# Kernel tuning notes

Hardware: AMD Instinct MI355X
Metric: run time of the kernel (lower is better)

Reference implementation:

```python
import jax, jax.numpy as jnp
import numpy as np

BS, N, E = 16, 1024, 262144
IN_DIM, HID, OUT, NREL, NBASES = 3072, 512, 128, 8, 4
N_LAYERS = 3


def setup_inputs() -> dict:
    key = jax.random.key(0)
    ks = jax.random.split(key, 10)
    tot = BS * N
    return {
        "h": jax.random.normal(ks[0], (BS, N, IN_DIM), jnp.float32),
        "src": jax.random.randint(ks[1], (E,), 0, tot, jnp.int32),
        "dst": jax.random.randint(ks[2], (E,), 0, tot, jnp.int32),
        "r": jax.random.randint(ks[3], (E,), 0, NREL, jnp.int32),
        "norm": jax.random.uniform(ks[4], (E,), jnp.float32),
        "W_elmo": jax.random.normal(ks[5], (IN_DIM, 256), jnp.float32) * 0.02,
        "b_elmo": jnp.zeros((256,), jnp.float32),
        "comp": jax.random.normal(ks[6], (NREL, NBASES), jnp.float32),
        "V": jax.random.normal(ks[7], (NBASES, HID, HID), jnp.float32) * 0.04,
        "b_gcn": jnp.zeros((HID,), jnp.float32),
        "W_out": jax.random.normal(ks[8], (HID, OUT), jnp.float32) * 0.04,
        "b_out": jnp.zeros((OUT,), jnp.float32),
    }


def reference(h, src, dst, r, norm, W_elmo, b_elmo, comp, V, b_gcn, W_out, b_out):
    bs, n, _ = h.shape
    tot = bs * n
    # elmo_fnn + relu, then concat with zeros -> gnn_h_dim = 512
    x = jax.nn.relu(h @ W_elmo + b_elmo)                 # [bs, N, 256]
    x = jnp.concatenate([x, jnp.zeros_like(x)], axis=-1)  # [bs, N, 512]
    x = x.reshape(tot, HID)                               # flattened batched-graph nodes

    coef = comp[r]  # [E, NBASES] per-edge relation coefficients (basis decomposition)
    nb = V.shape[0]
    for _ in range(N_LAYERS):  # shared RelGraphConv applied repeatedly
        hs = x[src]  # [E, HID] gather source node features per edge
        # message m_e = h_src @ (sum_b comp[r_e, b] * V_b); loop over small fixed basis count
        msg = coef[:, 0:1] * (hs @ V[0])
        for b in range(1, nb):
            msg = msg + coef[:, b:b + 1] * (hs @ V[b])
        msg = msg * norm[:, None]  # per-edge norm weighting
        x = jax.ops.segment_sum(msg, dst, num_segments=tot)  # scatter-aggregate to dst
        x = jax.nn.relu(x + b_gcn)  # bias + activation (no self-loop, dropout=0)

    x = x.reshape(bs, n, HID).mean(axis=1)  # mean over nodes per graph
    logits = x @ W_out + b_out
    return jax.nn.softmax(logits, axis=-1)
```

## Files before the change

kernel.cpp:

```cpp
#include <hip/hip_runtime.h>

typedef unsigned short u16;
typedef unsigned int   u32;
typedef u16   u16x4 __attribute__((ext_vector_type(4)));
typedef u16   u16x8 __attribute__((ext_vector_type(8)));
typedef short s16x8 __attribute__((ext_vector_type(8)));
typedef u32   u32x4 __attribute__((ext_vector_type(4)));
typedef float f32x4 __attribute__((ext_vector_type(4)));

__device__ __forceinline__ float bf2f(u16 u) {
    u32 x = ((u32)u) << 16;
    return __builtin_bit_cast(float, x);
}
__device__ __forceinline__ u16 f2bf(float f) {
    u32 u = __builtin_bit_cast(u32, f);
    u32 r = u + 0x7FFFu + ((u >> 16) & 1u);
    return (u16)(r >> 16);
}
__device__ __forceinline__ u32 cvtpk(float a, float b) {
    u32 r;
    asm("v_cvt_pk_bf16_f32 %0, %1, %2" : "=v"(r) : "v"(a), "v"(b));
    return r;
}

__device__ __forceinline__ void gload16(const void* g, void* lds) {
    __builtin_amdgcn_global_load_lds((const __attribute__((address_space(1))) void*)g,
                                     (__attribute__((address_space(3))) void*)lds, 16, 0, 0);
}

#define TOT   16384
#define HID   512
#define NRELS 8
#define EDGES 262144
#define INDIM 3072
#define NOUT  128
#define NGRAPH 16
#define NODESPER 1024
#define EKSPLIT 4

#define OFF_XB     ((size_t)0)
#define OFF_Y      (OFF_XB + 16777216)
#define OFF_WCT    (OFF_Y + 134217728)
#define OFF_WET    (OFF_WCT + 4194304)
#define OFF_CNT    (OFF_WET + 1572864)
#define OFF_ROWPTR (OFF_CNT + 65536)
#define OFF_CURSOR (OFF_ROWPTR + 65552)
#define OFF_EPK    (OFF_CURSOR + 65536)
#define OFF_ENORM  (OFF_EPK + 1048576)
#define OFF_PART   (OFF_ENORM + 1048576)

__global__ __launch_bounds__(256) void k_prep_wcat(const float* __restrict__ comp,
                                                   const float* __restrict__ V,
                                                   u16* __restrict__ WcatT) {
    __shared__ float tile[64][65];
    const int r = blockIdx.z, k0 = blockIdx.x * 64, n0 = blockIdx.y * 64;
    const float c0 = comp[r * 4], c1 = comp[r * 4 + 1], c2 = comp[r * 4 + 2], c3 = comp[r * 4 + 3];
    const int tn = threadIdx.x & 63;
    const int tk = threadIdx.x >> 6;
#pragma unroll
    for (int i = 0; i < 16; ++i) {
        int k = tk + i * 4;
        const float* vp = V + (size_t)(k0 + k) * 512 + n0 + tn;
        tile[k][tn] = c0 * vp[0] + c1 * vp[262144] + c2 * vp[2 * 262144] + c3 * vp[3 * 262144];
    }
    __syncthreads();
    const int kk = threadIdx.x & 63;
#pragma unroll
    for (int i = 0; i < 16; ++i) {
        int n = (threadIdx.x >> 6) + i * 4;
        WcatT[((size_t)(r * 512 + n0 + n) << 9) + k0 + kk] = f2bf(tile[kk][n]);
    }
}

__global__ __launch_bounds__(256) void k_prep_welmo(const float* __restrict__ W,
                                                    u16* __restrict__ WT) {
    __shared__ float tile[64][65];
    const int k0 = blockIdx.x * 64, n0 = blockIdx.y * 64;
    const int tn = threadIdx.x & 63;
    const int tk = threadIdx.x >> 6;
#pragma unroll
    for (int i = 0; i < 16; ++i) {
        int k = tk + i * 4;
        tile[k][tn] = W[(size_t)(k0 + k) * 256 + n0 + tn];
    }
    __syncthreads();
    const int kk = threadIdx.x & 63;
#pragma unroll
    for (int i = 0; i < 16; ++i) {
        int n = (threadIdx.x >> 6) + i * 4;
        WT[(size_t)(n0 + n) * 3072 + k0 + kk] = f2bf(tile[kk][n]);
    }
}

__global__ __launch_bounds__(256) void k_hist(const int* __restrict__ dst, int* __restrict__ cnt) {
    int e = blockIdx.x * 256 + threadIdx.x;
    atomicAdd(&cnt[dst[e]], 1);
}

__global__ __launch_bounds__(1024) void k_scan(const int* __restrict__ cnt,
                                               int* __restrict__ rowptr,
                                               int* __restrict__ cursor) {
    __shared__ int part[1024];
    int t = threadIdx.x;
    int loc[16];
    int s = 0;
    int base = t * 16;
#pragma unroll
    for (int i = 0; i < 16; ++i) { loc[i] = s; s += cnt[base + i]; }
    part[t] = s;
    __syncthreads();
    for (int off = 1; off < 1024; off <<= 1) {
        int v = (t >= off) ? part[t - off] : 0;
        __syncthreads();
        part[t] += v;
        __syncthreads();
    }
    int excl = (t == 0) ? 0 : part[t - 1];
#pragma unroll
    for (int i = 0; i < 16; ++i) {
        int v = excl + loc[i];
        rowptr[base + i] = v;
        cursor[base + i] = v;
    }
    if (t == 1023) rowptr[TOT] = part[1023];
}

__global__ __launch_bounds__(256) void k_scatter(const int* __restrict__ src,
                                                 const int* __restrict__ dst,
                                                 const int* __restrict__ rel,
                                                 const float* __restrict__ norm,
                                                 int* __restrict__ cursor,
                                                 int* __restrict__ epk,
                                                 float* __restrict__ enorm) {
    int e = blockIdx.x * 256 + threadIdx.x;
    int d = dst[e];
    int pos = atomicAdd(&cursor[d], 1);
    epk[pos] = (src[e] << 3) | rel[e];
    enorm[pos] = norm[e];
}

__global__ __launch_bounds__(256, 4) void k_gemm(const u16* __restrict__ A,
                                                 const u16* __restrict__ BT,
                                                 u16* __restrict__ C,
                                                 int K, int lda, int ldb, int ldc) {
    __shared__ __align__(16) u16 As[128 * 64];
    __shared__ __align__(16) u16 Bs[128 * 64];

    const int t = threadIdx.x;
    const int lin = blockIdx.y * 128 + blockIdx.x;
    const int swz = (lin & 7) * 512 + (lin >> 3);
    const int tileM = (swz & 127) * 128;
    const int tileN = (swz >> 7) * 128;

    const int w = t >> 6, l = t & 63;
    const int wr = w >> 1, wc = w & 1;
    const int lo = l & 15, hi = l >> 4;

    const int srow8 = l >> 3;
    const int scol = ((l & 7) ^ srow8) * 8;

    f32x4 acc[4][4];
#pragma unroll
    for (int m = 0; m < 4; ++m)
#pragma unroll
        for (int n = 0; n < 4; ++n) acc[m][n] = f32x4{0.f, 0.f, 0.f, 0.f};

    for (int k0 = 0; k0 < K; k0 += 64) {
#pragma unroll
        for (int i = 0; i < 4; ++i) {
            const int rowblk = (w * 4 + i) * 8;
            gload16(A + (size_t)(tileM + rowblk + srow8) * lda + k0 + scol, &As[rowblk * 64]);
            gload16(BT + (size_t)(tileN + rowblk + srow8) * ldb + k0 + scol, &Bs[rowblk * 64]);
        }
        __syncthreads();

#pragma unroll
        for (int kk = 0; kk < 2; ++kk) {
            s16x8 af[4], bf[4];
#pragma unroll
            for (int m = 0; m < 4; ++m) {
                int row = wr * 64 + m * 16 + lo;
                int boff = (row * 128 + kk * 64 + hi * 16) ^ ((row & 7) << 4);
                af[m] = *(const s16x8*)((const char*)As + boff);
            }
#pragma unroll
            for (int n = 0; n < 4; ++n) {
                int row = wc * 64 + n * 16 + lo;
                int boff = (row * 128 + kk * 64 + hi * 16) ^ ((row & 7) << 4);
                bf[n] = *(const s16x8*)((const char*)Bs + boff);
            }
#pragma unroll
            for (int m = 0; m < 4; ++m)
#pragma unroll
                for (int n = 0; n < 4; ++n)
                    acc[m][n] = __builtin_amdgcn_mfma_f32_16x16x32_bf16(
                        af[m], bf[n], acc[m][n], 0, 0, 0);
        }
        __syncthreads();
    }

#pragma unroll
    for (int m = 0; m < 4; ++m)
#pragma unroll
        for (int n = 0; n < 4; ++n) {
            int col = tileN + wc * 64 + n * 16 + lo;
#pragma unroll
            for (int j = 0; j < 4; ++j) {
                int row = tileM + wr * 64 + m * 16 + hi * 4 + j;
                C[(size_t)row * ldc + col] = f2bf(acc[m][n][j]);
            }
        }
}

__global__ __launch_bounds__(256, 2) void k_gemm_elmo(const float* __restrict__ A,
                                                      const u16* __restrict__ BT,
                                                      float* __restrict__ Cp) {
    __shared__ __align__(16) float As[128 * 64];
    __shared__ __align__(16) u16   Bs[256 * 64];

    const int t = threadIdx.x;
    const int tileM = blockIdx.x * 128;
    const int kz = blockIdx.y;
    const int kbeg = kz * (INDIM / EKSPLIT);

    const int w = t >> 6, l = t & 63;
    const int wr = w >> 1, wc = w & 1;
    const int lo = l & 15, hi = l >> 4;

    const int ar = l >> 4;
    const int br = l >> 3;
    const int bcol = ((l & 7) ^ br) * 8;

    f32x4 acc[4][8];
#pragma unroll
    for (int m = 0; m < 4; ++m)
#pragma unroll
        for (int n = 0; n < 8; ++n) acc[m][n] = f32x4{0.f, 0.f, 0.f, 0.f};

    for (int ks = 0; ks < 12; ++ks) {
        const int k0 = kbeg + ks * 64;
#pragma unroll
        for (int i = 0; i < 8; ++i) {
            const int RA = (w * 8 + i) * 4;
            const int ca = (l & 15) ^ ((RA & 15) + ar);
            gload16(A + (size_t)(tileM + RA + ar) * INDIM + k0 + ca * 4, &As[RA * 64]);
            const int RB = (w * 8 + i) * 8;
            gload16(BT + (size_t)(RB + br) * INDIM + k0 + bcol, &Bs[RB * 64]);
        }
        __syncthreads();

#pragma unroll
        for (int kk = 0; kk < 2; ++kk) {
            s16x8 afr[4], bfr[8];
#pragma unroll
            for (int m = 0; m < 4; ++m) {
                int ra = wr * 64 + m * 16 + lo;
                int x0 = kk * 8 + hi * 2;
                const char* base = (const char*)As + ra * 256;
                f32x4 p = *(const f32x4*)(base + (((x0) ^ (ra & 15)) << 4));
                f32x4 q = *(const f32x4*)(base + (((x0 + 1) ^ (ra & 15)) << 4));
                u32x4 pk = {cvtpk(p[0], p[1]), cvtpk(p[2], p[3]),
                            cvtpk(q[0], q[1]), cvtpk(q[2], q[3])};
                afr[m] = __builtin_bit_cast(s16x8, pk);
            }
#pragma unroll
            for (int n = 0; n < 8; ++n) {
                int rb = wc * 128 + n * 16 + lo;
                int boff = (rb * 128 + kk * 64 + hi * 16) ^ ((rb & 7) << 4);
                bfr[n] = *(const s16x8*)((const char*)Bs + boff);
            }
#pragma unroll
            for (int m = 0; m < 4; ++m)
#pragma unroll
                for (int n = 0; n < 8; ++n)
                    acc[m][n] = __builtin_amdgcn_mfma_f32_16x16x32_bf16(
                        afr[m], bfr[n], acc[m][n], 0, 0, 0);
        }
        __syncthreads();
    }

    float* cp = Cp + (size_t)kz * TOT * 256;
#pragma unroll
    for (int m = 0; m < 4; ++m)
#pragma unroll
        for (int n = 0; n < 8; ++n) {
            int col = wc * 128 + n * 16 + lo;
#pragma unroll
            for (int j = 0; j < 4; ++j) {
                int row = tileM + wr * 64 + m * 16 + hi * 4 + j;
                cp[(size_t)row * 256 + col] = acc[m][n][j];
            }
        }
}

__global__ __launch_bounds__(256) void k_elmo_reduce(const float* __restrict__ Cp,
                                                     const float* __restrict__ bias,
                                                     u16* __restrict__ xb) {
    int idx = blockIdx.x * 256 + threadIdx.x;
    int row = idx >> 6;
    int c4 = (idx & 63) * 4;
    f32x4 s = *(const f32x4*)(Cp + (size_t)row * 256 + c4);
#pragma unroll
    for (int p = 1; p < EKSPLIT; ++p)
        s += *(const f32x4*)(Cp + (size_t)p * TOT * 256 + (size_t)row * 256 + c4);
    f32x4 bv = *(const f32x4*)(bias + c4);
    u16x4 o;
#pragma unroll
    for (int j = 0; j < 4; ++j) o[j] = f2bf(fmaxf(s[j] + bv[j], 0.f));
    *(u16x4*)(xb + (size_t)row * HID + c4) = o;
}

__global__ __launch_bounds__(256) void k_agg(const u16* __restrict__ y,
                                             const int* __restrict__ rowptr,
                                             const int* __restrict__ epk,
                                             const float* __restrict__ enorm,
                                             const float* __restrict__ bgcn,
                                             u16* __restrict__ xout) {
    __shared__ int   s_epk[64];
    __shared__ float s_nrm[64];
    const int d = blockIdx.x, t = threadIdx.x;
    const u32* yw = (const u32*)y;

    float2 bv = *(const float2*)(bgcn + 2 * t);
    float a0 = bv.x, a1 = bv.y;

    const int beg = rowptr[d], end = rowptr[d + 1];
    for (int base = beg; base < end; base += 64) {
        const int m = min(64, end - base);
        if (t < m) { s_epk[t] = epk[base + t]; s_nrm[t] = enorm[base + t]; }
        __syncthreads();
        int c = 0;
        for (; c + 16 <= m; c += 16) {
            u32 wv[16];
            float nv[16];
#pragma unroll
            for (int q = 0; q < 16; ++q) {
                int k = s_epk[c + q];
                nv[q] = s_nrm[c + q];
                wv[q] = yw[((size_t)(k >> 3) << 11) + ((k & 7) << 8) + t];
            }
#pragma unroll
            for (int q = 0; q < 16; ++q) {
                a0 = fmaf(nv[q], bf2f((u16)wv[q]), a0);
                a1 = fmaf(nv[q], bf2f((u16)(wv[q] >> 16)), a1);
            }
        }
        for (; c + 4 <= m; c += 4) {
            u32 wv[4];
            float nv[4];
#pragma unroll
            for (int q = 0; q < 4; ++q) {
                int k = s_epk[c + q];
                nv[q] = s_nrm[c + q];
                wv[q] = yw[((size_t)(k >> 3) << 11) + ((k & 7) << 8) + t];
            }
#pragma unroll
            for (int q = 0; q < 4; ++q) {
                a0 = fmaf(nv[q], bf2f((u16)wv[q]), a0);
                a1 = fmaf(nv[q], bf2f((u16)(wv[q] >> 16)), a1);
            }
        }
        for (; c < m; ++c) {
            int k0 = s_epk[c];
            float n0 = s_nrm[c];
            u32 w0 = yw[((size_t)(k0 >> 3) << 11) + ((k0 & 7) << 8) + t];
            a0 = fmaf(n0, bf2f((u16)w0), a0);
            a1 = fmaf(n0, bf2f((u16)(w0 >> 16)), a1);
        }
        __syncthreads();
    }
    u32 o = (u32)f2bf(fmaxf(a0, 0.f)) | ((u32)f2bf(fmaxf(a1, 0.f)) << 16);
    ((u32*)xout)[((size_t)d << 8) + t] = o;
}

__global__ __launch_bounds__(512) void k_mean1(const u16* __restrict__ xb,
                                               float* __restrict__ part) {
    int g = blockIdx.x >> 4, chunk = blockIdx.x & 15, t = threadIdx.x;
    const u16* base = xb + ((size_t)g * NODESPER + chunk * 64) * HID;
    float s = 0.f;
    for (int n = 0; n < 64; ++n) s += bf2f(base[(size_t)n * HID + t]);
    part[(size_t)blockIdx.x * HID + t] = s;
}

__global__ __launch_bounds__(512) void k_final2(const float* __restrict__ part,
                                                const float* __restrict__ W_out,
                                                const float* __restrict__ b_out,
                                                float* __restrict__ out) {
    int g = blockIdx.x, t = threadIdx.x;
    __shared__ float mean_s[512];
    __shared__ float lg[128];
    __shared__ float red[128];
    float s = 0.f;
#pragma unroll
    for (int c = 0; c < 16; ++c) s += part[((size_t)g * 16 + c) * HID + t];
    mean_s[t] = s * (1.0f / (float)NODESPER);
    __syncthreads();
    if (t < NOUT) {
        float a = b_out[t];
        for (int k = 0; k < HID; ++k) a = fmaf(mean_s[k], W_out[(size_t)k * NOUT + t], a);
        lg[t] = a;
        red[t] = a;
    }
    __syncthreads();
    for (int off = 64; off > 0; off >>= 1) {
        if (t < off) red[t] = fmaxf(red[t], red[t + off]);
        __syncthreads();
    }
    float mx = red[0];
    __syncthreads();
    if (t < NOUT) { float e = expf(lg[t] - mx); lg[t] = e; red[t] = e; }
    __syncthreads();
    for (int off = 64; off > 0; off >>= 1) {
        if (t < off) red[t] += red[t + off];
        __syncthreads();
    }
    if (t < NOUT) out[(size_t)g * NOUT + t] = lg[t] / red[0];
}

extern "C" void kernel_launch(void* const* d_in, const int* in_sizes, int n_in,
                              void* d_out, int out_size, void* d_ws, size_t ws_size,
                              hipStream_t stream) {
    const float* h      = (const float*)d_in[0];
    const int*   src    = (const int*)d_in[1];
    const int*   dst    = (const int*)d_in[2];
    const int*   rel    = (const int*)d_in[3];
    const float* norm   = (const float*)d_in[4];
    const float* W_elmo = (const float*)d_in[5];
    const float* b_elmo = (const float*)d_in[6];
    const float* comp   = (const float*)d_in[7];
    const float* V      = (const float*)d_in[8];
    const float* b_gcn  = (const float*)d_in[9];
    const float* W_out  = (const float*)d_in[10];
    const float* b_out  = (const float*)d_in[11];
    float* out = (float*)d_out;

    char* ws = (char*)d_ws;
    u16*   xb     = (u16*)(ws + OFF_XB);
    u16*   y      = (u16*)(ws + OFF_Y);
    float* elmoP  = (float*)(ws + OFF_Y);
    u16*   wcatT  = (u16*)(ws + OFF_WCT);
    u16*   welmoT = (u16*)(ws + OFF_WET);
    int*   cnt    = (int*)(ws + OFF_CNT);
    int*   rowptr = (int*)(ws + OFF_ROWPTR);
    int*   cursor = (int*)(ws + OFF_CURSOR);
    int*   epk    = (int*)(ws + OFF_EPK);
    float* enorm  = (float*)(ws + OFF_ENORM);
    float* part   = (float*)(ws + OFF_PART);

    hipMemsetAsync(xb, 0, (size_t)TOT * HID * 2, stream);
    hipMemsetAsync(cnt, 0, (size_t)TOT * 4, stream);

    k_prep_wcat<<<dim3(8, 8, 8), 256, 0, stream>>>(comp, V, wcatT);
    k_prep_welmo<<<dim3(48, 4), 256, 0, stream>>>(W_elmo, welmoT);

    k_hist<<<EDGES / 256, 256, 0, stream>>>(dst, cnt);
    k_scan<<<1, 1024, 0, stream>>>(cnt, rowptr, cursor);
    k_scatter<<<EDGES / 256, 256, 0, stream>>>(src, dst, rel, norm, cursor, epk, enorm);

    k_gemm_elmo<<<dim3(128, EKSPLIT), 256, 0, stream>>>(h, welmoT, elmoP);
    k_elmo_reduce<<<4096, 256, 0, stream>>>(elmoP, b_elmo, xb);

    for (int L = 0; L < 3; ++L) {
        const int Keff = (L == 0) ? 256 : 512;
        k_gemm<<<dim3(128, 32), 256, 0, stream>>>(xb, wcatT, y, Keff, HID, HID,
                                                  NRELS * HID);
        k_agg<<<TOT, 256, 0, stream>>>(y, rowptr, epk, enorm, b_gcn, xb);
    }

    k_mean1<<<NGRAPH * 16, 512, 0, stream>>>(xb, part);
    k_final2<<<NGRAPH, 512, 0, stream>>>(part, W_out, b_out, out);
}
```

Baseline: 534.1 us.

## Triple-buffer GEMM K-loop and use wave-per-node vectorized aggregation

The relation GEMM now stages K in 32-wide slices across three LDS buffers, prefetching two slices ahead. It uses explicit vmcnt waits and a single barrier per step, and raises MFMA priority, so global loads overlap compute. The aggregation kernel maps one wavefront per destination node with 16-byte gathers per lane, replacing one block per node with LDS staging and block syncs. Occupancy bound drops from 4 to 3 blocks, and the per-node edge loop is now serial within a wave, with less memory-level parallelism per node.

Result: slower. 574.8 us (+7.6%).

```diff
diff --git a/kernel.cpp b/kernel.cpp
--- a/kernel.cpp
+++ b/kernel.cpp
@@ -139,12 +139,12 @@
     enorm[pos] = norm[e];
 }
 
-__global__ __launch_bounds__(256, 4) void k_gemm(const u16* __restrict__ A,
+__global__ __launch_bounds__(256, 3) void k_gemm(const u16* __restrict__ A,
                                                  const u16* __restrict__ BT,
                                                  u16* __restrict__ C,
                                                  int K, int lda, int ldb, int ldc) {
-    __shared__ __align__(16) u16 As[128 * 64];
-    __shared__ __align__(16) u16 Bs[128 * 64];
+    __shared__ __align__(16) u16 As[3][128 * 32];
+    __shared__ __align__(16) u16 Bs[3][128 * 32];
 
     const int t = threadIdx.x;
     const int lin = blockIdx.y * 128 + blockIdx.x;
@@ -156,8 +156,8 @@
     const int wr = w >> 1, wc = w & 1;
     const int lo = l & 15, hi = l >> 4;
 
-    const int srow8 = l >> 3;
-    const int scol = ((l & 7) ^ srow8) * 8;
+    const int sr = l >> 2;
+    const int sc = ((l & 3) ^ ((l >> 3) & 3)) * 8;
 
     f32x4 acc[4][4];
 #pragma unroll
@@ -165,39 +165,59 @@
 #pragma unroll
         for (int n = 0; n < 4; ++n) acc[m][n] = f32x4{0.f, 0.f, 0.f, 0.f};
 
-    for (int k0 = 0; k0 < K; k0 += 64) {
-#pragma unroll
-        for (int i = 0; i < 4; ++i) {
-            const int rowblk = (w * 4 + i) * 8;
-            gload16(A + (size_t)(tileM + rowblk + srow8) * lda + k0 + scol, &As[rowblk * 64]);
-            gload16(BT + (size_t)(tileN + rowblk + srow8) * ldb + k0 + scol, &Bs[rowblk * 64]);
-        }
-        __syncthreads();
-
-#pragma unroll
-        for (int kk = 0; kk < 2; ++kk) {
-            s16x8 af[4], bf[4];
-#pragma unroll
-            for (int m = 0; m < 4; ++m) {
-                int row = wr * 64 + m * 16 + lo;
-                int boff = (row * 128 + kk * 64 + hi * 16) ^ ((row & 7) << 4);
-                af[m] = *(const s16x8*)((const char*)As + boff);
-            }
-#pragma unroll
-            for (int n = 0; n < 4; ++n) {
-                int row = wc * 64 + n * 16 + lo;
-                int boff = (row * 128 + kk * 64 + hi * 16) ^ ((row & 7) << 4);
-                bf[n] = *(const s16x8*)((const char*)Bs + boff);
-            }
-#pragma unroll
-            for (int m = 0; m < 4; ++m)
-#pragma unroll
-                for (int n = 0; n < 4; ++n)
-                    acc[m][n] = __builtin_amdgcn_mfma_f32_16x16x32_bf16(
-                        af[m], bf[n], acc[m][n], 0, 0, 0);
-        }
-        __syncthreads();
-    }
+    const int nt = K >> 5;
+
+#define STG(pa, pb, ks)                                                              \
+    {                                                                                \
+        const int k0_ = (ks) * 32;                                                   \
+        _Pragma("unroll") for (int i = 0; i < 2; ++i) {                              \
+            const int rg = (w * 2 + i) * 16;                                         \
+            gload16(A + (size_t)(tileM + rg + sr) * lda + k0_ + sc, (pa) + rg * 32); \
+            gload16(BT + (size_t)(tileN + rg + sr) * ldb + k0_ + sc, (pb) + rg * 32);\
+        }                                                                            \
+    }
+
+    u16 *pa0 = &As[0][0], *pa1 = &As[1][0], *pa2 = &As[2][0];
+    u16 *pb0 = &Bs[0][0], *pb1 = &Bs[1][0], *pb2 = &Bs[2][0];
+
+    STG(pa0, pb0, 0);
+    STG(pa1, pb1, 1);
+
+    for (int tt = 0; tt < nt; ++tt) {
+        if (tt < nt - 1) asm volatile("s_waitcnt vmcnt(4)" ::: "memory");
+        else             asm volatile("s_waitcnt vmcnt(0)" ::: "memory");
+        __builtin_amdgcn_sched_barrier(0);
+        __builtin_amdgcn_s_barrier();
+        __builtin_amdgcn_sched_barrier(0);
+
+        if (tt + 2 < nt) STG(pa2, pb2, tt + 2);
+
+        const char* Ab = (const char*)pa0;
+        const char* Bb = (const char*)pb0;
+        s16x8 af[4], bf[4];
+#pragma unroll
+        for (int m = 0; m < 4; ++m) {
+            int ra = wr * 64 + m * 16 + lo;
+            af[m] = *(const s16x8*)(Ab + ra * 64 + ((hi ^ ((ra >> 1) & 3)) << 4));
+        }
+#pragma unroll
+        for (int n = 0; n < 4; ++n) {
+            int rb = wc * 64 + n * 16 + lo;
+            bf[n] = *(const s16x8*)(Bb + rb * 64 + ((hi ^ ((rb >> 1) & 3)) << 4));
+        }
+        __builtin_amdgcn_s_setprio(1);
+#pragma unroll
+        for (int m = 0; m < 4; ++m)
+#pragma unroll
+            for (int n = 0; n < 4; ++n)
+                acc[m][n] = __builtin_amdgcn_mfma_f32_16x16x32_bf16(
+                    af[m], bf[n], acc[m][n], 0, 0, 0);
+        __builtin_amdgcn_s_setprio(0);
+
+        u16* ta = pa0; pa0 = pa1; pa1 = pa2; pa2 = ta;
+        u16* tb = pb0; pb0 = pb1; pb1 = pb2; pb2 = tb;
+    }
+#undef STG
 
 #pragma unroll
     for (int m = 0; m < 4; ++m)
@@ -316,61 +336,54 @@
                                              const float* __restrict__ enorm,
                                              const float* __restrict__ bgcn,
                                              u16* __restrict__ xout) {
-    __shared__ int   s_epk[64];
-    __shared__ float s_nrm[64];
-    const int d = blockIdx.x, t = threadIdx.x;
-    const u32* yw = (const u32*)y;
-
-    float2 bv = *(const float2*)(bgcn + 2 * t);
-    float a0 = bv.x, a1 = bv.y;
-
-    const int beg = rowptr[d], end = rowptr[d + 1];
-    for (int base = beg; base < end; base += 64) {
-        const int m = min(64, end - base);
-        if (t < m) { s_epk[t] = epk[base + t]; s_nrm[t] = enorm[base + t]; }
-        __syncthreads();
-        int c = 0;
-        for (; c + 16 <= m; c += 16) {
-            u32 wv[16];
-            float nv[16];
-#pragma unroll
-            for (int q = 0; q < 16; ++q) {
-                int k = s_epk[c + q];
-                nv[q] = s_nrm[c + q];
-                wv[q] = yw[((size_t)(k >> 3) << 11) + ((k & 7) << 8) + t];
-            }
-#pragma unroll
-            for (int q = 0; q < 16; ++q) {
-                a0 = fmaf(nv[q], bf2f((u16)wv[q]), a0);
-                a1 = fmaf(nv[q], bf2f((u16)(wv[q] >> 16)), a1);
-            }
-        }
-        for (; c + 4 <= m; c += 4) {
-            u32 wv[4];
-            float nv[4];
-#pragma unroll
-            for (int q = 0; q < 4; ++q) {
-                int k = s_epk[c + q];
-                nv[q] = s_nrm[c + q];
-                wv[q] = yw[((size_t)(k >> 3) << 11) + ((k & 7) << 8) + t];
-            }
-#pragma unroll
-            for (int q = 0; q < 4; ++q) {
-                a0 = fmaf(nv[q], bf2f((u16)wv[q]), a0);
-                a1 = fmaf(nv[q], bf2f((u16)(wv[q] >> 16)), a1);
-            }
-        }
-        for (; c < m; ++c) {
-            int k0 = s_epk[c];
-            float n0 = s_nrm[c];
-            u32 w0 = yw[((size_t)(k0 >> 3) << 11) + ((k0 & 7) << 8) + t];
-            a0 = fmaf(n0, bf2f((u16)w0), a0);
-            a1 = fmaf(n0, bf2f((u16)(w0 >> 16)), a1);
-        }
-        __syncthreads();
-    }
-    u32 o = (u32)f2bf(fmaxf(a0, 0.f)) | ((u32)f2bf(fmaxf(a1, 0.f)) << 16);
-    ((u32*)xout)[((size_t)d << 8) + t] = o;
+    const int wid = (blockIdx.x * 256 + threadIdx.x) >> 6;
+    const int l = threadIdx.x & 63;
+    const u32x4* yv = (const u32x4*)y;
+
+    float a[8];
+    {
+        f32x4 b0 = *(const f32x4*)(bgcn + l * 8);
+        f32x4 b1 = *(const f32x4*)(bgcn + l * 8 + 4);
+#pragma unroll
+        for (int j = 0; j < 4; ++j) { a[j] = b0[j]; a[j + 4] = b1[j]; }
+    }
+
+    const int beg = rowptr[wid], end = rowptr[wid + 1];
+    int p = beg;
+    for (; p + 4 <= end; p += 4) {
+        int e0 = epk[p], e1 = epk[p + 1], e2 = epk[p + 2], e3 = epk[p + 3];
+        float n0 = enorm[p], n1 = enorm[p + 1], n2 = enorm[p + 2], n3 = enorm[p + 3];
+        u32x4 v0 = yv[(((size_t)(e0 >> 3)) << 9) + ((e0 & 7) << 6) + l];
+        u32x4 v1 = yv[(((size_t)(e1 >> 3)) << 9) + ((e1 & 7) << 6) + l];
+        u32x4 v2 = yv[(((size_t)(e2 >> 3)) << 9) + ((e2 & 7) << 6) + l];
+        u32x4 v3 = yv[(((size_t)(e3 >> 3)) << 9) + ((e3 & 7) << 6) + l];
+#pragma unroll
+        for (int q = 0; q < 4; ++q) {
+            a[2 * q]     = fmaf(n0, bf2f((u16)v0[q]), a[2 * q]);
+            a[2 * q + 1] = fmaf(n0, bf2f((u16)(v0[q] >> 16)), a[2 * q + 1]);
+            a[2 * q]     = fmaf(n1, bf2f((u16)v1[q]), a[2 * q]);
+            a[2 * q + 1] = fmaf(n1, bf2f((u16)(v1[q] >> 16)), a[2 * q + 1]);
+            a[2 * q]     = fmaf(n2, bf2f((u16)v2[q]), a[2 * q]);
+            a[2 * q + 1] = fmaf(n2, bf2f((u16)(v2[q] >> 16)), a[2 * q + 1]);
+            a[2 * q]     = fmaf(n3, bf2f((u16)v3[q]), a[2 * q]);
+            a[2 * q + 1] = fmaf(n3, bf2f((u16)(v3[q] >> 16)), a[2 * q + 1]);
+        }
+    }
+    for (; p < end; ++p) {
+        int e0 = epk[p];
+        float n0 = enorm[p];
+        u32x4 v0 = yv[(((size_t)(e0 >> 3)) << 9) + ((e0 & 7) << 6) + l];
+#pragma unroll
+        for (int q = 0; q < 4; ++q) {
+            a[2 * q]     = fmaf(n0, bf2f((u16)v0[q]), a[2 * q]);
+            a[2 * q + 1] = fmaf(n0, bf2f((u16)(v0[q] >> 16)), a[2 * q + 1]);
+        }
+    }
+
+    u16x8 o;
+#pragma unroll
+    for (int j = 0; j < 8; ++j) o[j] = f2bf(fmaxf(a[j], 0.f));
+    *(u16x8*)(xout + ((size_t)wid << 9) + l * 8) = o;
 }
 
 __global__ __launch_bounds__(512) void k_mean1(const u16* __restrict__ xb,
@@ -464,7 +477,7 @@
         const int Keff = (L == 0) ? 256 : 512;
         k_gemm<<<dim3(128, 32), 256, 0, stream>>>(xb, wcatT, y, Keff, HID, HID,
                                                   NRELS * HID);
-        k_agg<<<TOT, 256, 0, stream>>>(y, rowptr, epk, enorm, b_gcn, xb);
+        k_agg<<<TOT / 4, 256, 0, stream>>>(y, rowptr, epk, enorm, b_gcn, xb);
     }
 
     k_mean1<<<NGRAPH * 16, 512, 0, stream>>>(xb, part);
```
